# Performance work log

Hardware: AMD Instinct MI355X
Metric: run time of the kernel (lower is better)

Reference implementation:

```python
import jax, jax.numpy as jnp
import numpy as np

B, N, X, Y, W1, W2, D = 2, 6, 8, 8, 8, 8, 128
H, DH = 4, 32
L = X * Y          # number of windows
QT = N * W1 * W2   # tokens per window
EPS = 1e-5


def _ln(x, g, b):
    m = x.mean(-1, keepdims=True)
    v = ((x - m) ** 2).mean(-1, keepdims=True)
    return (x - m) * jax.lax.rsqrt(v + EPS) * g + b


def _win(t):
    # b n x y w1 w2 d -> b (x y) (n w1 w2) d
    return t.transpose(0, 2, 3, 1, 4, 5, 6).reshape(B, L, QT, D)


def setup_inputs() -> dict:
    key = jax.random.key(0)
    ks = jax.random.split(key, 12)
    s = 0.02
    inp = {
        'q': jax.random.normal(ks[0], (B, N, X, Y, W1, W2, D), jnp.float32),
        'k': jax.random.normal(ks[1], (B, N, X, Y, W1, W2, D), jnp.float32),
        'v': jax.random.normal(ks[2], (B, N, X, Y, W1, W2, D), jnp.float32),
        'skip': jax.random.normal(ks[3], (B, X, Y, W1, W2, D), jnp.float32),
        'gq': jnp.ones((D,), jnp.float32), 'betq': jnp.zeros((D,), jnp.float32),
        'gk': jnp.ones((D,), jnp.float32), 'betk': jnp.zeros((D,), jnp.float32),
        'gv': jnp.ones((D,), jnp.float32), 'betv': jnp.zeros((D,), jnp.float32),
        'wq': jax.random.normal(ks[4], (D, H * DH), jnp.float32) * s,
        'bq': jnp.zeros((H * DH,), jnp.float32),
        'wk': jax.random.normal(ks[5], (D, H * DH), jnp.float32) * s,
        'bk': jnp.zeros((H * DH,), jnp.float32),
        'wv': jax.random.normal(ks[6], (D, H * DH), jnp.float32) * s,
        'bv': jnp.zeros((H * DH,), jnp.float32),
        'wp': jax.random.normal(ks[7], (H * DH, D), jnp.float32) * s,
        'bp': jnp.zeros((D,), jnp.float32),
    }
    return inp


def reference(q, k, v, skip, gq, betq, gk, betk, gv, betv,
              wq, bq, wk, bk, wv, bv, wp, bp):
    scale = DH ** -0.5
    qw, kw, vw = _win(q), _win(k), _win(v)
    # LayerNorm + Linear QKV, split heads: (b, l, T, h, dh)
    qh = (_ln(qw, gq, betq) @ wq + bq).reshape(B, L, QT, H, DH)
    kh = (_ln(kw, gk, betk) @ wk + bk).reshape(B, L, QT, H, DH)
    vh = (_ln(vw, gv, betv) @ wv + bv).reshape(B, L, QT, H, DH)
    dot = scale * jnp.einsum('blqhd,blkhd->bhlqk', qh, kh)
    att = jax.nn.softmax(dot, axis=-1)
    a = jnp.einsum('bhlqk,blkhd->blqhd', att, vh).reshape(B, L, QT, H * DH)
    # b (x y) (n w1 w2) d -> b n x y w1 w2 d
    a = a.reshape(B, X, Y, N, W1, W2, H * DH).transpose(0, 3, 1, 2, 4, 5, 6)
    z = a @ wp + bp
    z = z.mean(1)  # average over views
    return z + skip
```

## Files before the change

kernel.cpp:

```cpp
#include <hip/hip_runtime.h>


typedef unsigned short u16;
typedef __bf16 bf16x8 __attribute__((ext_vector_type(8)));
typedef __bf16 bf16x4 __attribute__((ext_vector_type(4)));
typedef float  f32x16 __attribute__((ext_vector_type(16)));
typedef unsigned short u16x8 __attribute__((ext_vector_type(8)));

union U8 { u16x8 u; bf16x8 b; };

#if __has_builtin(__builtin_amdgcn_exp2f)
#define EXP2(x) __builtin_amdgcn_exp2f(x)
#else
#define EXP2(x) exp2f(x)
#endif

__device__ __forceinline__ f32x16 mfma_bf16(bf16x8 a, bf16x8 b, f32x16 c){
  return __builtin_amdgcn_mfma_f32_32x32x16_bf16(a, b, c, 0, 0, 0);
}


__global__ __launch_bounds__(512) void k_prep(
    const float* __restrict__ wq, const float* __restrict__ bq,
    const float* __restrict__ gq, const float* __restrict__ betq,
    const float* __restrict__ wk, const float* __restrict__ bk,
    const float* __restrict__ gk, const float* __restrict__ betk,
    const float* __restrict__ wv, const float* __restrict__ bv,
    const float* __restrict__ gv, const float* __restrict__ betv,
    const float* __restrict__ wp,
    u16* __restrict__ wqT, u16* __restrict__ wkT, u16* __restrict__ wvT, u16* __restrict__ wpT,
    float* __restrict__ bq2, float* __restrict__ bk2, float* __restrict__ bv2,
    float* __restrict__ uq2, float* __restrict__ uk2, float* __restrict__ uv2)
{
  __shared__ float wls[128*129];
  __shared__ float gls[128], bls[128];
  __shared__ float redb[512], redu[512];
  const float ALPHA_Q = 0.17677669529663687f * 1.4426950408889634f;
  int wsel = blockIdx.x, tid = threadIdx.x;
  const float *w, *bb, *g, *bet; u16* wT; float *b2, *u2; float alpha;
  if (wsel == 0){ w=wq; bb=bq; g=gq; bet=betq; wT=wqT; b2=bq2; u2=uq2; alpha=ALPHA_Q; }
  else if (wsel == 1){ w=wk; bb=bk; g=gk; bet=betk; wT=wkT; b2=bk2; u2=uk2; alpha=1.f; }
  else if (wsel == 2){ w=wv; bb=bv; g=gv; bet=betv; wT=wvT; b2=bv2; u2=uv2; alpha=1.f; }
  else { w=wp; bb=nullptr; g=nullptr; bet=nullptr; wT=wpT; b2=nullptr; u2=nullptr; alpha=1.f; }

  if (tid < 128){
    gls[tid] = g ? g[tid] : 1.f;
    bls[tid] = bet ? bet[tid] : 0.f;
  }
  const float4* w4 = (const float4*)w;
  #pragma unroll
  for (int i = 0; i < 8; i++){
    int idx = tid + i*512;
    int row = idx >> 5, c4 = (idx & 31) * 4;
    float4 x = w4[idx];
    wls[row*129 + c4 + 0] = x.x;
    wls[row*129 + c4 + 1] = x.y;
    wls[row*129 + c4 + 2] = x.z;
    wls[row*129 + c4 + 3] = x.w;
  }
  __syncthreads();
  int n = tid >> 2, qp = tid & 3;
  float sb = 0.f, su = 0.f;
  alignas(16) __bf16 tmp[32];
  #pragma unroll
  for (int kk = 0; kk < 32; kk++){
    int k2 = qp*32 + kk;
    float wv_ = wls[k2*129 + n];
    float gv_ = gls[k2];
    sb += bls[k2] * wv_;
    su += gv_ * wv_;
    tmp[kk] = (__bf16)(wv_ * gv_ * alpha);
  }
  #pragma unroll
  for (int j = 0; j < 4; j++)
    *(bf16x8*)(wT + n*128 + qp*32 + j*8) = *(bf16x8*)&tmp[j*8];
  redb[tid] = sb; redu[tid] = su;
  __syncthreads();
  if (qp == 0 && bb){
    float s = bb[n] + redb[tid] + redb[tid+1] + redb[tid+2] + redb[tid+3];
    float u = redu[tid] + redu[tid+1] + redu[tid+2] + redu[tid+3];
    b2[n] = s * alpha;
    u2[n] = u * alpha;
  }
}

__global__ __launch_bounds__(256) void k_lnproj(
    const float* __restrict__ qg, const float* __restrict__ kg, const float* __restrict__ vg,
    const u16* __restrict__ wqT, const u16* __restrict__ wkT, const u16* __restrict__ wvT,
    const float* __restrict__ bq2, const float* __restrict__ bk2, const float* __restrict__ bv2,
    const float* __restrict__ uq2, const float* __restrict__ uk2, const float* __restrict__ uv2,
    u16* __restrict__ qh, u16* __restrict__ kh, u16* __restrict__ vh)
{
  __shared__ alignas(16) u16 Abf[64*136];
  __shared__ float s1s[64], s2s[64];
  int bid = blockIdx.x, tid = threadIdx.x;
  int which = bid % 3;
  int t = bid / 3;
  int n = t % 6, bl = t / 6;
  const float* src; const u16* wT; const float *b2, *u2; u16* dstb;
  if (which == 0){ src=qg; wT=wqT; b2=bq2; u2=uq2; dstb=qh; }
  else if (which == 1){ src=kg; wT=wkT; b2=bk2; u2=uk2; dstb=kh; }
  else { src=vg; wT=wvT; b2=bv2; u2=uv2; dstb=vh; }
  int b = bl >> 6, l = bl & 63;
  const float4* s4 = (const float4*)(src + (size_t)((b*6 + n)*64 + l)*64*128);
  #pragma unroll
  for (int i = 0; i < 8; i++){
    int idx = tid + i*256;
    int row = idx >> 5, c4 = idx & 31;
    float4 xv = s4[idx];
    float s1 = xv.x + xv.y + xv.z + xv.w;
    float s2 = xv.x*xv.x + xv.y*xv.y + xv.z*xv.z + xv.w*xv.w;
    #pragma unroll
    for (int m = 1; m < 32; m <<= 1){
      s1 += __shfl_xor(s1, m, 64);
      s2 += __shfl_xor(s2, m, 64);
    }
    if (c4 == 0){ s1s[row] = s1; s2s[row] = s2; }
    bf16x4 pk;
    pk[0] = (__bf16)xv.x; pk[1] = (__bf16)xv.y;
    pk[2] = (__bf16)xv.z; pk[3] = (__bf16)xv.w;
    *(bf16x4*)&Abf[row*136 + c4*4] = pk;
  }
  __syncthreads();
  if (tid < 64){
    float m = s1s[tid] * (1.f/128.f);
    float r = rsqrtf(s2s[tid] * (1.f/128.f) - m*m + 1e-5f);
    s1s[tid] = r;
    s2s[tid] = r * m;
  }
  int wave = tid >> 6, lane = tid & 63, lm = lane & 31, lh = lane >> 5;
  bf16x8 bfr[8];
  const u16* wrow = wT + (32*wave + lm)*128 + lh*8;
  #pragma unroll
  for (int ks = 0; ks < 8; ks++) bfr[ks] = *(const bf16x8*)(wrow + ks*16);
  f32x16 acc0, acc1;
  #pragma unroll
  for (int r = 0; r < 16; r++){ acc0[r]=0.f; acc1[r]=0.f; }
  #pragma unroll
  for (int ks = 0; ks < 8; ks++){
    bf16x8 a0 = *(const bf16x8*)&Abf[lm*136       + ks*16 + lh*8];
    bf16x8 a1 = *(const bf16x8*)&Abf[(32+lm)*136  + ks*16 + lh*8];
    acc0 = mfma_bf16(a0, bfr[ks], acc0);
    acc1 = mfma_bf16(a1, bfr[ks], acc1);
  }
  __syncthreads();
  int col = 32*wave + lm;
  float u2c = u2[col], bc = b2[col];
  u16* dst = dstb + ((size_t)(bl*4 + wave)*384 + n*64)*32 + lm;
  #pragma unroll
  for (int r = 0; r < 16; r++){
    int row0 = (r&3) + 8*(r>>2) + 4*lh;
    float y0 = s1s[row0]     * acc0[r] - s2s[row0]     * u2c + bc;
    float y1 = s1s[row0+32]  * acc1[r] - s2s[row0+32]  * u2c + bc;
    *(__bf16*)&dst[(size_t)row0*32]      = (__bf16)y0;
    *(__bf16*)&dst[(size_t)(32+row0)*32] = (__bf16)y1;
  }
}

__global__ __launch_bounds__(768, 6) void k_attn(
    const u16* __restrict__ qh, const u16* __restrict__ kh, const u16* __restrict__ vh,
    u16* __restrict__ abar)
{
  __shared__ alignas(16) u16 vts[32*408];
  __shared__ float abar_s[64*32];
  int bid = blockIdx.x, tid = threadIdx.x;
  int h = bid & 3, bl = bid >> 2;
  const u16* qb = qh + (size_t)bid * (384*32);
  const u16* kb = kh + (size_t)bid * (384*32);
  const u16* vb = vh + (size_t)bid * (384*32);

  #pragma unroll
  for (int i = 0; i < 2; i++){
    int c = tid + i*768;
    int key = c >> 2, part = c & 3;
    int u = key & 31, tt = key >> 5;
    int a = u >> 2;
    int anew = (a & 4) | ((a & 1) << 1) | ((a >> 1) & 1);
    int pos = tt*32 + anew*4 + (u & 3);
    u16x8 vv = *(const u16x8*)(vb + key*32 + part*8);
    #pragma unroll
    for (int j = 0; j < 8; j++) vts[(part*8 + j)*408 + pos] = vv[j];
  }
  for (int idx = tid; idx < 2048; idx += 768) abar_s[idx] = 0.f;
  __syncthreads();

  int wave = tid >> 6, lane = tid & 63, lm = lane & 31, lh = lane >> 5;
  int n = wave >> 1, qoff = (wave & 1) * 32;
  int qrow = n*64 + qoff + lm;

  bf16x8 qf0 = *(const bf16x8*)(qb + qrow*32 +      lh*8);
  bf16x8 qf1 = *(const bf16x8*)(qb + qrow*32 + 16 + lh*8);

  f32x16 oacc;
  #pragma unroll
  for (int r = 0; r < 16; r++) oacc[r] = 0.f;
  float sle = 0.f;

  const u16* vrow = &vts[lm*408 + 8*lh];

  for (int kt = 0; kt < 12; kt++){
    int K0 = kt*32;
    bf16x8 kf0 = *(const bf16x8*)(kb + (K0+lm)*32 +      lh*8);
    bf16x8 kf1 = *(const bf16x8*)(kb + (K0+lm)*32 + 16 + lh*8);
    f32x16 s;
    #pragma unroll
    for (int r = 0; r < 16; r++) s[r] = 0.f;
    s = mfma_bf16(kf0, qf0, s);
    s = mfma_bf16(kf1, qf1, s);
    U8 p0, p1;
    #pragma unroll
    for (int r = 0; r < 8; r++){
      float e0 = EXP2(s[r]);
      float e1 = EXP2(s[r+8]);
      sle += e0 + e1;
      p0.b[r] = (__bf16)e0;
      p1.b[r] = (__bf16)e1;
    }
    U8 vb0, vb1;
    vb0.u = *(const u16x8*)(vrow + K0);
    vb1.u = *(const u16x8*)(vrow + K0 + 16);
    oacc = mfma_bf16(p0.b, vb0.b, oacc);
    oacc = mfma_bf16(p1.b, vb1.b, oacc);
  }

  sle += __shfl_xor(sle, 32, 64);
  float inv = (1.f/6.f) / sle;

  #pragma unroll
  for (int r = 0; r < 16; r++){
    int q_l = (r&3) + 8*(r>>2) + 4*lh;
    float o = oacc[r] * __shfl(inv, q_l, 64);
    atomicAdd(&abar_s[(qoff + q_l)*32 + lm], o);
  }
  __syncthreads();
  u16* ob = abar + (size_t)(bl*64)*128 + h*32;
  for (int idx = tid; idx < 2048; idx += 768){
    int w12 = idx >> 5, dh = idx & 31;
    *(__bf16*)&ob[(size_t)w12*128 + dh] = (__bf16)abar_s[idx];
  }
}

__global__ __launch_bounds__(256) void k_out(
    const u16* __restrict__ abar, const u16* __restrict__ wpT,
    const float* __restrict__ bp, const float* __restrict__ skip,
    float* __restrict__ out)
{
  __shared__ alignas(16) u16 Als[64*136];
  int tid = threadIdx.x;
  int R0 = blockIdx.x * 64;
  #pragma unroll
  for (int i = 0; i < 4; i++){
    int c = tid + i*256;
    int row = c >> 4, part = c & 15;
    *(u16x8*)&Als[row*136 + part*8] = *(const u16x8*)(abar + (size_t)(R0+row)*128 + part*8);
  }
  __syncthreads();
  int wave = tid >> 6, lane = tid & 63, lm = lane & 31, lh = lane >> 5;
  bf16x8 bfr[8];
  const u16* wrow = wpT + (32*wave + lm)*128 + lh*8;
  #pragma unroll
  for (int ks = 0; ks < 8; ks++) bfr[ks] = *(const bf16x8*)(wrow + ks*16);
  f32x16 acc0, acc1;
  #pragma unroll
  for (int r = 0; r < 16; r++){ acc0[r]=0.f; acc1[r]=0.f; }
  #pragma unroll
  for (int ks = 0; ks < 8; ks++){
    bf16x8 a0 = *(const bf16x8*)&Als[lm*136      + ks*16 + lh*8];
    bf16x8 a1 = *(const bf16x8*)&Als[(32+lm)*136 + ks*16 + lh*8];
    acc0 = mfma_bf16(a0, bfr[ks], acc0);
    acc1 = mfma_bf16(a1, bfr[ks], acc1);
  }
  float bias = bp[32*wave + lm];
  #pragma unroll
  for (int r = 0; r < 16; r++){
    int row0 = (r&3) + 8*(r>>2) + 4*lh;
    size_t f0 = (size_t)(R0 + row0)*128 + 32*wave + lm;
    out[f0] = acc0[r] + bias + skip[f0];
    size_t f1 = (size_t)(R0 + 32 + row0)*128 + 32*wave + lm;
    out[f1] = acc1[r] + bias + skip[f1];
  }
}

extern "C" void kernel_launch(void* const* d_in, const int* in_sizes, int n_in,
                              void* d_out, int out_size, void* d_ws, size_t ws_size,
                              hipStream_t stream)
{
  const float* q    = (const float*)d_in[0];
  const float* k    = (const float*)d_in[1];
  const float* v    = (const float*)d_in[2];
  const float* skip = (const float*)d_in[3];
  const float* gq   = (const float*)d_in[4];
  const float* betq = (const float*)d_in[5];
  const float* gk   = (const float*)d_in[6];
  const float* betk = (const float*)d_in[7];
  const float* gv   = (const float*)d_in[8];
  const float* betv = (const float*)d_in[9];
  const float* wq   = (const float*)d_in[10];
  const float* bq   = (const float*)d_in[11];
  const float* wk   = (const float*)d_in[12];
  const float* bk   = (const float*)d_in[13];
  const float* wv   = (const float*)d_in[14];
  const float* bv   = (const float*)d_in[15];
  const float* wp   = (const float*)d_in[16];
  const float* bp   = (const float*)d_in[17];
  float* out = (float*)d_out;

  char* ws = (char*)d_ws;
  u16* wqT = (u16*)ws;
  u16* wkT = wqT + 16384;
  u16* wvT = wkT + 16384;
  u16* wpT = wvT + 16384;
  float* bq2 = (float*)(ws + 131072);
  float* bk2 = bq2 + 128;
  float* bv2 = bk2 + 128;
  float* uq2 = bv2 + 128;
  float* uk2 = uq2 + 128;
  float* uv2 = uk2 + 128;
  u16* qh = (u16*)(ws + 134144);
  u16* kh = qh + 6291456;
  u16* vh = kh + 6291456;
  u16* abar = vh + 6291456;

  k_prep  <<<4,    512, 0, stream>>>(wq,bq,gq,betq, wk,bk,gk,betk, wv,bv,gv,betv, wp,
                                     wqT,wkT,wvT,wpT, bq2,bk2,bv2, uq2,uk2,uv2);
  k_lnproj<<<2304, 256, 0, stream>>>(q,k,v, wqT,wkT,wvT, bq2,bk2,bv2, uq2,uk2,uv2, qh,kh,vh);
  k_attn  <<<512,  768, 0, stream>>>(qh,kh,vh, abar);
  k_out   <<<128,  256, 0, stream>>>(abar, wpT, bp, skip, out);
}
```

Measured before the change: 221.4 us.

## Prefetch K/V fragments in attention loop and simplify LayerNorm stats reduction

The attention kernel now double-buffers the K global loads and the V LDS reads, fetching tile kt+1 while tile kt is computed, and it hoists the Q/K fragment loads ahead of the V transpose into shared memory. The projection kernel changes its row mapping so that four threads own one row. Each thread accumulates its partial sums across the loop and needs only a two-step shuffle, which removes one __syncthreads and the single-thread stats pass. This hides load latency at the cost of more registers, and the new row-contiguous load pattern may coalesce less well.

```diff
diff --git a/kernel.cpp b/kernel.cpp
--- a/kernel.cpp
+++ b/kernel.cpp
@@ -103,31 +103,27 @@
   else { src=vg; wT=wvT; b2=bv2; u2=uv2; dstb=vh; }
   int b = bl >> 6, l = bl & 63;
   const float4* s4 = (const float4*)(src + (size_t)((b*6 + n)*64 + l)*64*128);
+  int row = tid >> 2, j = tid & 3;
+  float s1 = 0.f, s2 = 0.f;
   #pragma unroll
   for (int i = 0; i < 8; i++){
-    int idx = tid + i*256;
-    int row = idx >> 5, c4 = idx & 31;
-    float4 xv = s4[idx];
-    float s1 = xv.x + xv.y + xv.z + xv.w;
-    float s2 = xv.x*xv.x + xv.y*xv.y + xv.z*xv.z + xv.w*xv.w;
-    #pragma unroll
-    for (int m = 1; m < 32; m <<= 1){
-      s1 += __shfl_xor(s1, m, 64);
-      s2 += __shfl_xor(s2, m, 64);
-    }
-    if (c4 == 0){ s1s[row] = s1; s2s[row] = s2; }
+    float4 xv = s4[row*32 + i*4 + j];
+    s1 += xv.x + xv.y + xv.z + xv.w;
+    s2 += xv.x*xv.x + xv.y*xv.y + xv.z*xv.z + xv.w*xv.w;
     bf16x4 pk;
     pk[0] = (__bf16)xv.x; pk[1] = (__bf16)xv.y;
     pk[2] = (__bf16)xv.z; pk[3] = (__bf16)xv.w;
-    *(bf16x4*)&Abf[row*136 + c4*4] = pk;
-  }
-  __syncthreads();
-  if (tid < 64){
-    float m = s1s[tid] * (1.f/128.f);
-    float r = rsqrtf(s2s[tid] * (1.f/128.f) - m*m + 1e-5f);
-    s1s[tid] = r;
-    s2s[tid] = r * m;
-  }
+    *(bf16x4*)&Abf[row*136 + (i*4 + j)*4] = pk;
+  }
+  s1 += __shfl_xor(s1, 1, 64); s1 += __shfl_xor(s1, 2, 64);
+  s2 += __shfl_xor(s2, 1, 64); s2 += __shfl_xor(s2, 2, 64);
+  if (j == 0){
+    float m = s1 * (1.f/128.f);
+    float r = rsqrtf(s2 * (1.f/128.f) - m*m + 1e-5f);
+    s1s[row] = r;
+    s2s[row] = r * m;
+  }
+  __syncthreads();
   int wave = tid >> 6, lane = tid & 63, lm = lane & 31, lh = lane >> 5;
   bf16x8 bfr[8];
   const u16* wrow = wT + (32*wave + lm)*128 + lh*8;
@@ -143,7 +139,6 @@
     acc0 = mfma_bf16(a0, bfr[ks], acc0);
     acc1 = mfma_bf16(a1, bfr[ks], acc1);
   }
-  __syncthreads();
   int col = 32*wave + lm;
   float u2c = u2[col], bc = b2[col];
   u16* dst = dstb + ((size_t)(bl*4 + wave)*384 + n*64)*32 + lm;
@@ -168,6 +163,16 @@
   const u16* qb = qh + (size_t)bid * (384*32);
   const u16* kb = kh + (size_t)bid * (384*32);
   const u16* vb = vh + (size_t)bid * (384*32);
+
+  int wave = tid >> 6, lane = tid & 63, lm = lane & 31, lh = lane >> 5;
+  int n = wave >> 1, qoff = (wave & 1) * 32;
+  int qrow = n*64 + qoff + lm;
+
+  bf16x8 qf0 = *(const bf16x8*)(qb + qrow*32 +      lh*8);
+  bf16x8 qf1 = *(const bf16x8*)(qb + qrow*32 + 16 + lh*8);
+  bf16x8 kf0[2], kf1[2];
+  kf0[0] = *(const bf16x8*)(kb + lm*32 +      lh*8);
+  kf1[0] = *(const bf16x8*)(kb + lm*32 + 16 + lh*8);
 
   #pragma unroll
   for (int i = 0; i < 2; i++){
@@ -179,34 +184,36 @@
     int pos = tt*32 + anew*4 + (u & 3);
     u16x8 vv = *(const u16x8*)(vb + key*32 + part*8);
     #pragma unroll
-    for (int j = 0; j < 8; j++) vts[(part*8 + j)*408 + pos] = vv[j];
+    for (int jj = 0; jj < 8; jj++) vts[(part*8 + jj)*408 + pos] = vv[jj];
   }
   for (int idx = tid; idx < 2048; idx += 768) abar_s[idx] = 0.f;
   __syncthreads();
 
-  int wave = tid >> 6, lane = tid & 63, lm = lane & 31, lh = lane >> 5;
-  int n = wave >> 1, qoff = (wave & 1) * 32;
-  int qrow = n*64 + qoff + lm;
-
-  bf16x8 qf0 = *(const bf16x8*)(qb + qrow*32 +      lh*8);
-  bf16x8 qf1 = *(const bf16x8*)(qb + qrow*32 + 16 + lh*8);
+  const u16* vrow = &vts[lm*408 + 8*lh];
+  U8 v0[2], v1[2];
+  v0[0].u = *(const u16x8*)(vrow);
+  v1[0].u = *(const u16x8*)(vrow + 16);
 
   f32x16 oacc;
   #pragma unroll
   for (int r = 0; r < 16; r++) oacc[r] = 0.f;
   float sle = 0.f;
 
-  const u16* vrow = &vts[lm*408 + 8*lh];
-
+  #pragma unroll
   for (int kt = 0; kt < 12; kt++){
-    int K0 = kt*32;
-    bf16x8 kf0 = *(const bf16x8*)(kb + (K0+lm)*32 +      lh*8);
-    bf16x8 kf1 = *(const bf16x8*)(kb + (K0+lm)*32 + 16 + lh*8);
+    int cur = kt & 1, nxt = cur ^ 1;
+    if (kt < 11){
+      int K1 = (kt+1)*32;
+      kf0[nxt] = *(const bf16x8*)(kb + (K1+lm)*32 +      lh*8);
+      kf1[nxt] = *(const bf16x8*)(kb + (K1+lm)*32 + 16 + lh*8);
+      v0[nxt].u = *(const u16x8*)(vrow + K1);
+      v1[nxt].u = *(const u16x8*)(vrow + K1 + 16);
+    }
     f32x16 s;
     #pragma unroll
     for (int r = 0; r < 16; r++) s[r] = 0.f;
-    s = mfma_bf16(kf0, qf0, s);
-    s = mfma_bf16(kf1, qf1, s);
+    s = mfma_bf16(kf0[cur], qf0, s);
+    s = mfma_bf16(kf1[cur], qf1, s);
     U8 p0, p1;
     #pragma unroll
     for (int r = 0; r < 8; r++){
@@ -216,11 +223,8 @@
       p0.b[r] = (__bf16)e0;
       p1.b[r] = (__bf16)e1;
     }
-    U8 vb0, vb1;
-    vb0.u = *(const u16x8*)(vrow + K0);
-    vb1.u = *(const u16x8*)(vrow + K0 + 16);
-    oacc = mfma_bf16(p0.b, vb0.b, oacc);
-    oacc = mfma_bf16(p1.b, vb1.b, oacc);
+    oacc = mfma_bf16(p0.b, v0[cur].b, oacc);
+    oacc = mfma_bf16(p1.b, v1[cur].b, oacc);
   }
 
   sle += __shfl_xor(sle, 32, 64);
```

Result: no change. 221.3 us (-0.1%).
